# Kernel tuning notes

Measured on AMD Instinct MI355X. Metric: run time of the kernel, lower is better.

The kernel has to match this reference:

```python
import jax, jax.numpy as jnp
import numpy as np

N, E, G = 40000, 400000, 64
IN, ED, HID, HEADS, OUT = 2, 18, 64, 4, 3

def _glorot(key, shape):
    fan_in = shape[0]
    return jax.random.normal(key, shape, dtype=jnp.float32) / np.float32(np.sqrt(fan_in))

def setup_inputs():
    key = jax.random.key(0)
    ks = jax.random.split(key, 32)
    d1 = HEADS * HID  # 256
    return {
        "x": jax.random.normal(ks[0], (N, IN), jnp.float32),
        "edge_index": jax.random.randint(ks[1], (2, E), 0, N),
        "edge_attr": jax.random.normal(ks[2], (E, ED), jnp.float32),
        "batch": jnp.sort(jax.random.randint(ks[3], (N,), 0, G)),
        # conv1: TransformerConv(2 -> 64, heads=4, concat=True, beta=True, edge_dim=18)
        "Wq1": _glorot(ks[4], (IN, d1)), "bq1": jnp.zeros((d1,), jnp.float32),
        "Wk1": _glorot(ks[5], (IN, d1)), "bk1": jnp.zeros((d1,), jnp.float32),
        "Wv1": _glorot(ks[6], (IN, d1)), "bv1": jnp.zeros((d1,), jnp.float32),
        "We1": _glorot(ks[7], (ED, d1)),
        "Wskip1": _glorot(ks[8], (IN, d1)), "bskip1": jnp.zeros((d1,), jnp.float32),
        "Wbeta1": _glorot(ks[9], (3 * d1, 1)),
        # conv2: TransformerConv(256 -> 64, heads=1, concat=False, beta=True, edge_dim=18)
        "Wq2": _glorot(ks[10], (d1, HID)), "bq2": jnp.zeros((HID,), jnp.float32),
        "Wk2": _glorot(ks[11], (d1, HID)), "bk2": jnp.zeros((HID,), jnp.float32),
        "Wv2": _glorot(ks[12], (d1, HID)), "bv2": jnp.zeros((HID,), jnp.float32),
        "We2": _glorot(ks[13], (ED, HID)),
        "Wskip2": _glorot(ks[14], (d1, HID)), "bskip2": jnp.zeros((HID,), jnp.float32),
        "Wbeta2": _glorot(ks[15], (3 * HID, 1)),
        "Wlin": _glorot(ks[16], (HID, OUT)), "blin": jnp.zeros((OUT,), jnp.float32),
    }

def _tconv(x, src, dst, edge_attr, Wq, bq, Wk, bk, Wv, bv, We, Wskip, bskip, Wbeta, H, C, concat):
    # PyG TransformerConv with edge_dim, beta=True, root_weight=True (eval: dropout off)
    n = x.shape[0]
    q = (x @ Wq + bq).reshape(n, H, C)
    k = (x @ Wk + bk).reshape(n, H, C)
    v = (x @ Wv + bv).reshape(n, H, C)
    e = (edge_attr @ We).reshape(-1, H, C)              # [E,H,C]
    kj = k[src] + e                                      # key_j + edge
    alpha = jnp.einsum('ehc,ehc->eh', q[dst], kj) * (1.0 / (C ** 0.5))  # [E,H]
    # segment softmax over destination nodes
    amax = jax.ops.segment_max(alpha, dst, num_segments=n)
    ex = jnp.exp(alpha - amax[dst])
    den = jax.ops.segment_sum(ex, dst, num_segments=n)
    w = ex / (den[dst] + 1e-16)
    msg = (v[src] + e) * w[:, :, None]                   # [E,H,C]
    out = jax.ops.segment_sum(msg, dst, num_segments=n)  # [N,H,C]
    out = out.reshape(n, H * C) if concat else out.mean(axis=1)
    # beta-gated skip connection
    xr = x @ Wskip + bskip
    beta = jax.nn.sigmoid(jnp.concatenate([out, xr, out - xr], axis=-1) @ Wbeta)
    return beta * xr + (1.0 - beta) * out

def reference(x, edge_index, edge_attr, batch, Wq1, bq1, Wk1, bk1, Wv1, bv1, We1, Wskip1, bskip1, Wbeta1, Wq2, bq2, Wk2, bk2, Wv2, bv2, We2, Wskip2, bskip2, Wbeta2, Wlin, blin):
    src, dst = edge_index[0], edge_index[1]
    h = jax.nn.relu(_tconv(x, src, dst, edge_attr, Wq1, bq1, Wk1, bk1, Wv1, bv1, We1, Wskip1, bskip1, Wbeta1, HEADS, HID, True))
    h = jax.nn.relu(_tconv(h, src, dst, edge_attr, Wq2, bq2, Wk2, bk2, Wv2, bv2, We2, Wskip2, bskip2, Wbeta2, 1, HID, False))
    # global mean pool per graph
    s = jax.ops.segment_sum(h, batch, num_segments=G)
    cnt = jax.ops.segment_sum(jnp.ones((h.shape[0], 1), h.dtype), batch, num_segments=G)
    pooled = s / jnp.maximum(cnt, 1.0)
    return pooled @ Wlin + blin
```

## Files before the change

### kernel.cpp

```cpp
#include <hip/hip_runtime.h>
#include <hip/hip_fp16.h>

#define N_NODES 40000
#define N_EDGES 400000
#define N_GRAPHS 64
#define D1 256
#define HIDC 64
#define NHEADS 4
#define EDIM 18
#define EPADH 24
#define OUTF 3
#define APAD 264

typedef _Float16 f16x8 __attribute__((ext_vector_type(8)));
typedef float f32x4 __attribute__((ext_vector_type(4)));

__global__ void prep_w(const float* __restrict__ Wq, const float* __restrict__ bq,
                       const float* __restrict__ Wk, const float* __restrict__ bk,
                       const float* __restrict__ Wv, const float* __restrict__ bv,
                       const float* __restrict__ Ws, const float* __restrict__ bs,
                       const float* __restrict__ We2,
                       const float* __restrict__ Wq1, const float* __restrict__ bq1,
                       const float* __restrict__ Wk1, const float* __restrict__ bk1,
                       const float* __restrict__ We1,
                       __half* __restrict__ Bt, float* __restrict__ bias,
                       float* __restrict__ cbuf, int* __restrict__ deg) {
    int c = blockIdx.x, k = threadIdx.x;
    int gid = c * 256 + k;
    if (gid < N_NODES) deg[gid] = 0;
    if (c < 256) {
        int m = c >> 6, d = c & 63;
        const float* W = (m == 0) ? Wq : (m == 1) ? Wk : (m == 2) ? Wv : Ws;
        Bt[c * 256 + k] = __float2half(W[k * 64 + d]);
        if (k == 0) {
            const float* b = (m == 0) ? bq : (m == 1) ? bk : (m == 2) ? bv : bs;
            bias[c] = b[d];
        }
    } else if (c < 288) {
        int j = c - 256;
        float s = 0.f;
        if (j < EDIM)
            for (int cc = 0; cc < 64; ++cc) s += Wq[k * 64 + cc] * We2[j * 64 + cc];
        Bt[c * 256 + k] = __float2half(s);
        if (k == 0) {
            float b = 0.f;
            if (j < EDIM)
                for (int cc = 0; cc < 64; ++cc) b += bq[cc] * We2[j * 64 + cc];
            bias[c] = b;
        }
    } else {
        int t = k;
        if (t < 36) {
            int h = t / 9, r = t % 9, a = r / 3, b = r % 3;
            const float* A = (a == 0) ? Wq1 : (a == 1) ? Wq1 + D1 : bq1;
            const float* B = (b == 0) ? Wk1 : (b == 1) ? Wk1 + D1 : bk1;
            float s = 0.f;
            for (int cc = 0; cc < 64; ++cc) s += A[h * 64 + cc] * B[h * 64 + cc];
            cbuf[h * 63 + a * 3 + b] = s;
        } else if (t < 252) {
            int i = t - 36;
            int h = i / 54, rr = (i % 54) / 18, j = i % 18;
            const float* A = (rr == 0) ? Wq1 : (rr == 1) ? Wq1 + D1 : bq1;
            float s = 0.f;
            for (int cc = 0; cc < 64; ++cc) s += A[h * 64 + cc] * We1[j * D1 + h * 64 + cc];
            cbuf[h * 63 + 9 + rr * 18 + j] = s;
        }
    }
}

__global__ void initA(const float* __restrict__ x, const float* __restrict__ cbuf,
                      const int* __restrict__ ei, const int* __restrict__ batch,
                      float* __restrict__ coef, float* __restrict__ acc1,
                      float* __restrict__ acc2, float* __restrict__ out2,
                      int* __restrict__ deg, float* __restrict__ pooled,
                      int* __restrict__ gs, int* __restrict__ ge) {
    int t = blockIdx.x * 256 + threadIdx.x;
    acc1[t] = 0.f;
    {
        int n = t / 84, r = t % 84, h = r / 21, c = r % 21;
        const float* cb = cbuf + h * 63;
        float x0 = x[2 * n], x1 = x[2 * n + 1], o;
        if (c < 3) o = x0 * cb[c] + x1 * cb[3 + c] + cb[6 + c];
        else { int j = c - 3; o = x0 * cb[9 + j] + x1 * cb[27 + j] + cb[45 + j]; }
        coef[t] = o;
    }
    if (t < N_NODES * 64) out2[t] = 0.f;
    if (t < N_NODES * 20) acc2[t] = 0.f;
    if (t < N_EDGES) atomicAdd(&deg[ei[N_EDGES + t]], 1);
    if (t < N_GRAPHS * HIDC) pooled[t] = 0.f;
    if (t < N_NODES) {
        int b = batch[t];
        if (t == 0) gs[b] = 0;
        else { int pb = batch[t - 1]; if (pb != b) { ge[pb] = t; gs[b] = t; } }
        if (t == N_NODES - 1) ge[b] = N_NODES;
    }
}

__global__ void scanA(const int* __restrict__ deg, int* __restrict__ bsum) {
    __shared__ int s[256];
    int b = blockIdx.x, t = threadIdx.x;
    s[t] = (t < 160) ? deg[b * 160 + t] : 0;
    __syncthreads();
    for (int off = 128; off; off >>= 1) {
        if (t < off) s[t] += s[t + off];
        __syncthreads();
    }
    if (t == 0) bsum[b] = s[0];
}

__global__ void scanB(const int* __restrict__ bsum, int* __restrict__ boff) {
    __shared__ int s[256];
    int t = threadIdx.x;
    int v = (t < 250) ? bsum[t] : 0;
    s[t] = v;
    __syncthreads();
    for (int off = 1; off < 256; off <<= 1) {
        int add = (t >= off) ? s[t - off] : 0;
        __syncthreads();
        s[t] += add;
        __syncthreads();
    }
    if (t < 250) boff[t] = s[t] - v;
}

__global__ void scanC(const int* __restrict__ deg, const int* __restrict__ boff,
                      int* __restrict__ cursor) {
    __shared__ int s[256];
    int b = blockIdx.x, t = threadIdx.x;
    int v = (t < 160) ? deg[b * 160 + t] : 0;
    s[t] = v;
    __syncthreads();
    for (int off = 1; off < 256; off <<= 1) {
        int add = (t >= off) ? s[t - off] : 0;
        __syncthreads();
        s[t] += add;
        __syncthreads();
    }
    if (t < 160) cursor[b * 160 + t] = boff[b] + s[t] - v;
}

__global__ void perm_kernel(const int* __restrict__ ei, int* __restrict__ cursor,
                            int* __restrict__ inv) {
    int e = blockIdx.x * 256 + threadIdx.x;
    if (e >= N_EDGES) return;
    int p = atomicAdd(&cursor[ei[N_EDGES + e]], 1);
    inv[p] = e;
}

__global__ void gatherE(const int* __restrict__ inv, const int* __restrict__ ei,
                        const float* __restrict__ ea, const float* __restrict__ x,
                        const float* __restrict__ coef,
                        int* __restrict__ src_s, int* __restrict__ dst_s,
                        _Float16* __restrict__ eah, float* __restrict__ alpha1) {
    int p = blockIdx.x * 256 + threadIdx.x;
    if (p >= N_EDGES) return;
    int e = inv[p];
    int src = ei[e], dst = ei[N_EDGES + e];
    src_s[p] = src;
    dst_s[p] = dst;
    const float* srow = ea + (size_t)e * EDIM;
    float s[EDIM];
    #pragma unroll
    for (int j = 0; j < EDIM; ++j) s[j] = srow[j];
    float x0 = x[src * 2], x1 = x[src * 2 + 1];
    f16x8 r0 = {(_Float16)s[0], (_Float16)s[1], (_Float16)s[2], (_Float16)s[3],
                (_Float16)s[4], (_Float16)s[5], (_Float16)s[6], (_Float16)s[7]};
    f16x8 r1 = {(_Float16)s[8], (_Float16)s[9], (_Float16)s[10], (_Float16)s[11],
                (_Float16)s[12], (_Float16)s[13], (_Float16)s[14], (_Float16)s[15]};
    f16x8 r2 = {(_Float16)s[16], (_Float16)s[17], (_Float16)x0, (_Float16)x1,
                (_Float16)0.f, (_Float16)0.f, (_Float16)0.f, (_Float16)0.f};
    _Float16* drow = eah + (size_t)p * EPADH;
    *(f16x8*)(drow)      = r0;
    *(f16x8*)(drow + 8)  = r1;
    *(f16x8*)(drow + 16) = r2;
    const float* cb = coef + (size_t)dst * 84;
    #pragma unroll
    for (int h = 0; h < NHEADS; ++h) {
        const float* c = cb + h * 21;
        float a = x0 * c[0] + x1 * c[1] + c[2];
        #pragma unroll
        for (int j = 0; j < EDIM; ++j) a += s[j] * c[3 + j];
        alpha1[(size_t)h * N_EDGES + p] = __expf(a * 0.125f);
    }
}

__global__ void strip1(const int* __restrict__ dst_s, const float* __restrict__ alpha1,
                       const _Float16* __restrict__ eah, float* __restrict__ acc1) {
    int t = threadIdx.x;
    int strip = blockIdx.x * 2 + (t >> 7);
    int gl = t & 127;
    bool active = gl < 84;
    int cgl = active ? gl : 83;
    int h = cgl / 21, comp = cgl % 21;
    int voff = (comp == 0) ? 18 : (comp == 1) ? 19 : (comp - 3);
    bool isone = (comp == 2);
    int p0 = strip * 16;
    int dsts[16]; float w[16]; float v[16];
    #pragma unroll
    for (int j = 0; j < 16; ++j) dsts[j] = dst_s[p0 + j];
    #pragma unroll
    for (int j = 0; j < 16; ++j) w[j] = alpha1[(size_t)h * N_EDGES + p0 + j];
    #pragma unroll
    for (int j = 0; j < 16; ++j)
        v[j] = isone ? 1.f : (float)eah[(size_t)(p0 + j) * EPADH + voff];
    float acc = 0.f;
    int prev = dsts[0];
    #pragma unroll
    for (int j = 0; j < 16; ++j) {
        if (dsts[j] != prev) {
            if (active) atomicAdd(&acc1[(size_t)prev * 84 + gl], acc);
            acc = 0.f; prev = dsts[j];
        }
        acc += w[j] * v[j];
    }
    if (active) atomicAdd(&acc1[(size_t)prev * 84 + gl], acc);
}

__global__ void finalize1x(const float* __restrict__ x, const float* __restrict__ acc1,
                           const float* __restrict__ Wv, const float* __restrict__ bv,
                           const float* __restrict__ We, const float* __restrict__ Wskip,
                           const float* __restrict__ bskip, const float* __restrict__ Wbeta,
                           __half* __restrict__ h1f) {
    __shared__ float red[4][4];
    int nb = blockIdx.x * 4;
    int t = threadIdx.x;
    int h = t >> 6;
    float wv0 = Wv[t], wv1 = Wv[D1 + t], bvv = bv[t];
    float we[EDIM];
    #pragma unroll
    for (int j = 0; j < EDIM; ++j) we[j] = We[j * D1 + t];
    float ws0 = Wskip[t], ws1 = Wskip[D1 + t], bsv = bskip[t];
    float wb0 = Wbeta[t], wb1 = Wbeta[D1 + t], wb2 = Wbeta[2 * D1 + t];
    float o[4], xr[4], part[4];
    #pragma unroll
    for (int i = 0; i < 4; ++i) {
        int node = nb + i;
        const float* a = acc1 + (size_t)node * 84 + h * 21;
        float l = a[2];
        float oo = a[0] * wv0 + a[1] * wv1 + l * bvv;
        #pragma unroll
        for (int j = 0; j < EDIM; ++j) oo += a[3 + j] * we[j];
        oo /= (l + 1e-16f);
        float x0 = x[node * 2], x1 = x[node * 2 + 1];
        xr[i] = x0 * ws0 + x1 * ws1 + bsv;
        o[i] = oo;
        part[i] = oo * wb0 + xr[i] * wb1 + (oo - xr[i]) * wb2;
    }
    #pragma unroll
    for (int off = 32; off; off >>= 1) {
        #pragma unroll
        for (int i = 0; i < 4; ++i) part[i] += __shfl_xor(part[i], off);
    }
    if ((t & 63) == 0) {
        #pragma unroll
        for (int i = 0; i < 4; ++i) red[h][i] = part[i];
    }
    __syncthreads();
    #pragma unroll
    for (int i = 0; i < 4; ++i) {
        float tot = red[0][i] + red[1][i] + red[2][i] + red[3][i];
        float beta = 1.f / (1.f + __expf(-tot));
        h1f[(size_t)(nb + i) * D1 + t] =
            __float2half(fmaxf(beta * xr[i] + (1.f - beta) * o[i], 0.f));
    }
}

__device__ __forceinline__ void nl2_store(int c, int gr, float v,
        float* __restrict__ q2, float* __restrict__ k2, __half* __restrict__ v2h,
        float* __restrict__ xr2, float* __restrict__ qe) {
    if (c < 256) {
        int m = c >> 6, d = c & 63;
        if (m == 0)      q2[(size_t)gr * 64 + d] = v;
        else if (m == 1) k2[(size_t)gr * 64 + d] = v;
        else if (m == 2) v2h[(size_t)gr * 64 + d] = __float2half(v);
        else             xr2[(size_t)gr * 64 + d] = v;
    } else {
        qe[(size_t)gr * 32 + (c - 256)] = v;
    }
}

__global__ __launch_bounds__(256) void nl2_mfma(
        const __half* __restrict__ h1f, const __half* __restrict__ Bt,
        const float* __restrict__ bias,
        float* __restrict__ q2, float* __restrict__ k2,
        __half* __restrict__ v2h, float* __restrict__ xr2,
        float* __restrict__ qe) {
    __shared__ _Float16 As[64 * APAD];
    int t = threadIdx.x;
    int row0 = blockIdx.x * 64;
    const float4* gsrc = (const float4*)(h1f + (size_t)row0 * 256);
    #pragma unroll
    for (int i = 0; i < 8; ++i) {
        int li = i * 256 + t;
        int r = li >> 5, c8 = li & 31;
        *(float4*)(As + r * APAD + c8 * 8) = gsrc[li];
    }
    __syncthreads();
    int wave = t >> 6, lane = t & 63, quad = lane >> 4, mm = lane & 15;
    const _Float16* Bp = (const _Float16*)Bt;
    for (int ct = wave; ct < 18; ct += 4) {
        int c0 = ct * 16 + mm;
        const _Float16* b0 = Bp + (size_t)c0 * 256 + quad * 8;
        f16x8 b[8];
        #pragma unroll
        for (int s = 0; s < 8; ++s) b[s] = *(const f16x8*)(b0 + s * 32);
        float bz = bias[c0];
        #pragma unroll
        for (int rt = 0; rt < 4; ++rt) {
            const _Float16* arow = As + (rt * 16 + mm) * APAD + quad * 8;
            f16x8 a[8];
            #pragma unroll
            for (int s = 0; s < 8; ++s) a[s] = *(const f16x8*)(arow + s * 32);
            f32x4 accA = {bz, bz, bz, bz};
            f32x4 accB = {0.f, 0.f, 0.f, 0.f};
            #pragma unroll
            for (int s = 0; s < 4; ++s) {
                accA = __builtin_amdgcn_mfma_f32_16x16x32_f16(a[s],     b[s],     accA, 0, 0, 0);
                accB = __builtin_amdgcn_mfma_f32_16x16x32_f16(a[s + 4], b[s + 4], accB, 0, 0, 0);
            }
            #pragma unroll
            for (int r = 0; r < 4; ++r) {
                int gr = row0 + rt * 16 + quad * 4 + r;
                nl2_store(c0, gr, accA[r] + accB[r], q2, k2, v2h, xr2, qe);
            }
        }
    }
}

#define LG2_BLOCKS 2048
#define LG2_WAVES (LG2_BLOCKS * 4)
__global__ void logits2(const int* __restrict__ src_s, const int* __restrict__ dst_s,
                        const _Float16* __restrict__ eah, const float* __restrict__ q2,
                        const float* __restrict__ k2, const float* __restrict__ qe,
                        float* __restrict__ alpha2) {
    int t = threadIdx.x, wid = t >> 6, lane = t & 63;
    int w = blockIdx.x * 4 + wid;
    for (int base = w; base < N_EDGES; base += 2 * LG2_WAVES) {
        int p1 = base, p2 = base + LG2_WAVES;
        bool has2 = p2 < N_EDGES;
        int p2c = has2 ? p2 : p1;
        int s1 = src_s[p1], d1 = dst_s[p1];
        int s2 = src_s[p2c], d2 = dst_s[p2c];
        float dd1 = q2[(size_t)d1 * 64 + lane] * k2[(size_t)s1 * 64 + lane];
        float dd2 = q2[(size_t)d2 * 64 + lane] * k2[(size_t)s2 * 64 + lane];
        if (lane < EDIM) {
            dd1 += qe[(size_t)d1 * 32 + lane] * (float)eah[(size_t)p1 * EPADH + lane];
            dd2 += qe[(size_t)d2 * 32 + lane] * (float)eah[(size_t)p2c * EPADH + lane];
        }
        #pragma unroll
        for (int off = 32; off; off >>= 1) {
            dd1 += __shfl_xor(dd1, off);
            dd2 += __shfl_xor(dd2, off);
        }
        if (lane == 0) {
            alpha2[p1] = __expf(dd1 * 0.125f);
            if (has2) alpha2[p2] = __expf(dd2 * 0.125f);
        }
    }
}

__global__ void spmm2s(const int* __restrict__ dst_s, const int* __restrict__ src_s,
                       const float* __restrict__ alpha2, const __half* __restrict__ v2h,
                       const _Float16* __restrict__ eah,
                       float* __restrict__ out2, float* __restrict__ acc2) {
    int t = threadIdx.x;
    int strip = blockIdx.x * 4 + (t >> 6);
    int lane = t & 63;
    int p0 = strip * 16;
    int dsts[16]; int srcs[16]; float w[16];
    #pragma unroll
    for (int j = 0; j < 16; ++j) dsts[j] = dst_s[p0 + j];
    #pragma unroll
    for (int j = 0; j < 16; ++j) srcs[j] = src_s[p0 + j];
    #pragma unroll
    for (int j = 0; j < 16; ++j) w[j] = alpha2[p0 + j];
    float vv[16]; float ev[16];
    #pragma unroll
    for (int j = 0; j < 16; ++j) vv[j] = __half2float(v2h[(size_t)srcs[j] * 64 + lane]);
    #pragma unroll
    for (int j = 0; j < 16; ++j)
        ev[j] = (lane < EDIM) ? (float)eah[(size_t)(p0 + j) * EPADH + lane] : 1.f;
    float acc = 0.f, accS = 0.f;
    int prev = dsts[0];
    #pragma unroll
    for (int j = 0; j < 16; ++j) {
        if (dsts[j] != prev) {
            atomicAdd(&out2[(size_t)prev * 64 + lane], acc);
            if (lane < 19) atomicAdd(&acc2[(size_t)prev * 20 + lane], accS);
            acc = 0.f; accS = 0.f; prev = dsts[j];
        }
        acc += w[j] * vv[j];
        accS += w[j] * ev[j];
    }
    atomicAdd(&out2[(size_t)prev * 64 + lane], acc);
    if (lane < 19) atomicAdd(&acc2[(size_t)prev * 20 + lane], accS);
}

__global__ void finalize2x(const float* __restrict__ out2, const float* __restrict__ acc2,
                           const float* __restrict__ xr2, const float* __restrict__ We2,
                           const float* __restrict__ Wb2, float* __restrict__ h2) {
    __shared__ float w2s[EDIM * 64];
    int t = threadIdx.x;
    for (int i = t; i < EDIM * 64; i += 256) w2s[i] = We2[i];
    __syncthreads();
    int node = blockIdx.x * 4 + (t >> 6);
    int lane = t & 63;
    const float* a2 = acc2 + (size_t)node * 20;
    float num = out2[(size_t)node * 64 + lane];
    #pragma unroll
    for (int j = 0; j < EDIM; ++j) num += a2[j] * w2s[j * 64 + lane];
    float o = num / (a2[18] + 1e-16f);
    float xr = xr2[(size_t)node * 64 + lane];
    float part = o * Wb2[lane] + xr * Wb2[64 + lane] + (o - xr) * Wb2[128 + lane];
    #pragma unroll
    for (int off = 32; off; off >>= 1) part += __shfl_xor(part, off);
    float beta = 1.f / (1.f + __expf(-part));
    h2[(size_t)node * 64 + lane] = fmaxf(beta * xr + (1.f - beta) * o, 0.f);
}

__global__ void pool_kernel(const float* __restrict__ h2, const int* __restrict__ gs,
                            const int* __restrict__ ge, float* __restrict__ pooled) {
    __shared__ float red[4][64];
    int g = blockIdx.x >> 2, q = blockIdx.x & 3;
    int t = threadIdx.x, wv = t >> 6, lane = t & 63;
    int s = gs[g], e = ge[g];
    float sum = 0.f;
    for (int n = s + q * 4 + wv; n < e; n += 16) sum += h2[(size_t)n * 64 + lane];
    red[wv][lane] = sum;
    __syncthreads();
    if (wv == 0) {
        float v = red[0][lane] + red[1][lane] + red[2][lane] + red[3][lane];
        atomicAdd(&pooled[g * 64 + lane], v);
    }
}

__global__ void final_lin(const float* __restrict__ pooled, const int* __restrict__ gs,
                          const int* __restrict__ ge,
                          const float* __restrict__ Wlin, const float* __restrict__ blin,
                          float* __restrict__ out) {
    int t = threadIdx.x;
    if (t >= N_GRAPHS * OUTF) return;
    int g = t / OUTF, o = t % OUTF;
    int c = ge[g] - gs[g];
    float inv = 1.f / fmaxf((float)c, 1.f);
    float acc = 0.f;
    for (int kk = 0; kk < HIDC; ++kk) acc += pooled[g * 64 + kk] * Wlin[kk * OUTF + o];
    out[t] = acc * inv + blin[o];
}

extern "C" void kernel_launch(void* const* d_in, const int* in_sizes, int n_in,
                              void* d_out, int out_size, void* d_ws, size_t ws_size,
                              hipStream_t stream) {
    const float* x      = (const float*)d_in[0];
    const int*   ei     = (const int*)d_in[1];
    const float* ea     = (const float*)d_in[2];
    const int*   batch  = (const int*)d_in[3];
    const float* Wq1    = (const float*)d_in[4];  const float* bq1    = (const float*)d_in[5];
    const float* Wk1    = (const float*)d_in[6];  const float* bk1    = (const float*)d_in[7];
    const float* Wv1    = (const float*)d_in[8];  const float* bv1    = (const float*)d_in[9];
    const float* We1    = (const float*)d_in[10];
    const float* Wskip1 = (const float*)d_in[11]; const float* bskip1 = (const float*)d_in[12];
    const float* Wbeta1 = (const float*)d_in[13];
    const float* Wq2    = (const float*)d_in[14]; const float* bq2    = (const float*)d_in[15];
    const float* Wk2    = (const float*)d_in[16]; const float* bk2    = (const float*)d_in[17];
    const float* Wv2    = (const float*)d_in[18]; const float* bv2    = (const float*)d_in[19];
    const float* We2    = (const float*)d_in[20];
    const float* Wskip2 = (const float*)d_in[21]; const float* bskip2 = (const float*)d_in[22];
    const float* Wbeta2 = (const float*)d_in[23];
    const float* Wlin   = (const float*)d_in[24]; const float* blin   = (const float*)d_in[25];

    float* ptr = (float*)d_ws;
    float* q2     = ptr; ptr += (size_t)N_NODES * 64;
    float* k2     = ptr; ptr += (size_t)N_NODES * 64;
    float* xr2    = ptr; ptr += (size_t)N_NODES * 64;
    float* qe     = ptr; ptr += (size_t)N_NODES * 32;
    __half* v2h   = (__half*)ptr; ptr += (size_t)N_NODES * 32;
    _Float16* eah = (_Float16*)ptr; ptr += (size_t)N_EDGES * EPADH / 2;
    float* alpha2 = ptr; ptr += N_EDGES;
    float* acc2   = ptr; ptr += (size_t)N_NODES * 20;
    float* out2   = ptr; ptr += (size_t)N_NODES * 64;
    float* pooled = ptr; ptr += N_GRAPHS * HIDC;
    int*   gs     = (int*)ptr; ptr += N_GRAPHS;
    int*   ge     = (int*)ptr; ptr += N_GRAPHS;
    float* cbuf   = ptr; ptr += 256;
    float* bias   = ptr; ptr += 320;
    __half* Bt    = (__half*)ptr; ptr += (288 * 256) / 2;
    int*   src_s  = (int*)ptr; ptr += N_EDGES;
    int*   dst_s  = (int*)ptr; ptr += N_EDGES;
    int*   inv    = (int*)ptr; ptr += N_EDGES;
    int*   deg    = (int*)ptr; ptr += N_NODES;
    int*   cursor = (int*)ptr; ptr += N_NODES;
    int*   bsum   = (int*)ptr; ptr += 256;
    int*   boff   = (int*)ptr; ptr += 256;
    float* coef   = ptr; ptr += (size_t)N_NODES * 84;
    float* h2     = coef;
    float* acc1   = ptr; ptr += (size_t)N_NODES * 84;
    float* alpha1 = ptr; ptr += (size_t)4 * N_EDGES;
    __half* h1f   = (__half*)ptr; ptr += (size_t)N_NODES * 128;

    const int EB = (N_EDGES + 255) / 256;

    prep_w<<<289, 256, 0, stream>>>(Wq2, bq2, Wk2, bk2, Wv2, bv2, Wskip2, bskip2, We2,
                                    Wq1, bq1, Wk1, bk1, We1, Bt, bias, cbuf, deg);
    initA<<<(N_NODES * 84) / 256, 256, 0, stream>>>(x, cbuf, ei, batch, coef, acc1,
                                                    acc2, out2, deg, pooled, gs, ge);
    scanA<<<250, 256, 0, stream>>>(deg, bsum);
    scanB<<<1, 256, 0, stream>>>(bsum, boff);
    scanC<<<250, 256, 0, stream>>>(deg, boff, cursor);
    perm_kernel<<<EB, 256, 0, stream>>>(ei, cursor, inv);
    gatherE<<<EB, 256, 0, stream>>>(inv, ei, ea, x, coef, src_s, dst_s, eah, alpha1);

    strip1<<<(N_EDGES / 16) / 2, 256, 0, stream>>>(dst_s, alpha1, eah, acc1);
    finalize1x<<<N_NODES / 4, 256, 0, stream>>>(x, acc1, Wv1, bv1, We1, Wskip1, bskip1,
                                                Wbeta1, h1f);

    nl2_mfma<<<N_NODES / 64, 256, 0, stream>>>(h1f, Bt, bias, q2, k2, v2h, xr2, qe);
    logits2<<<LG2_BLOCKS, 256, 0, stream>>>(src_s, dst_s, eah, q2, k2, qe, alpha2);
    spmm2s<<<(N_EDGES / 16) / 4, 256, 0, stream>>>(dst_s, src_s, alpha2, v2h, eah,
                                                   out2, acc2);
    finalize2x<<<N_NODES / 4, 256, 0, stream>>>(out2, acc2, xr2, We2, Wbeta2, h2);

    pool_kernel<<<N_GRAPHS * 4, 256, 0, stream>>>(h2, gs, ge, pooled);
    final_lin<<<1, 256, 0, stream>>>(pooled, gs, ge, Wlin, blin, (float*)d_out);
}
```

Baseline: 457.0 us.

## Fuse edge permutation into scatter kernel and double strip length in SpMM kernels

```diff
diff --git a/kernel.cpp b/kernel.cpp
--- a/kernel.cpp
+++ b/kernel.cpp
@@ -139,23 +139,15 @@
     if (t < 160) cursor[b * 160 + t] = boff[b] + s[t] - v;
 }
 
-__global__ void perm_kernel(const int* __restrict__ ei, int* __restrict__ cursor,
-                            int* __restrict__ inv) {
+__global__ void scatterE(const int* __restrict__ ei, const float* __restrict__ ea,
+                         const float* __restrict__ x, const float* __restrict__ coef,
+                         int* __restrict__ cursor,
+                         int* __restrict__ src_s, int* __restrict__ dst_s,
+                         _Float16* __restrict__ eah, float* __restrict__ alpha1) {
     int e = blockIdx.x * 256 + threadIdx.x;
     if (e >= N_EDGES) return;
-    int p = atomicAdd(&cursor[ei[N_EDGES + e]], 1);
-    inv[p] = e;
-}
-
-__global__ void gatherE(const int* __restrict__ inv, const int* __restrict__ ei,
-                        const float* __restrict__ ea, const float* __restrict__ x,
-                        const float* __restrict__ coef,
-                        int* __restrict__ src_s, int* __restrict__ dst_s,
-                        _Float16* __restrict__ eah, float* __restrict__ alpha1) {
-    int p = blockIdx.x * 256 + threadIdx.x;
-    if (p >= N_EDGES) return;
-    int e = inv[p];
     int src = ei[e], dst = ei[N_EDGES + e];
+    int p = atomicAdd(&cursor[dst], 1);
     src_s[p] = src;
     dst_s[p] = dst;
     const float* srow = ea + (size_t)e * EDIM;
@@ -194,24 +186,28 @@
     int h = cgl / 21, comp = cgl % 21;
     int voff = (comp == 0) ? 18 : (comp == 1) ? 19 : (comp - 3);
     bool isone = (comp == 2);
-    int p0 = strip * 16;
-    int dsts[16]; float w[16]; float v[16];
-    #pragma unroll
-    for (int j = 0; j < 16; ++j) dsts[j] = dst_s[p0 + j];
-    #pragma unroll
-    for (int j = 0; j < 16; ++j) w[j] = alpha1[(size_t)h * N_EDGES + p0 + j];
-    #pragma unroll
-    for (int j = 0; j < 16; ++j)
-        v[j] = isone ? 1.f : (float)eah[(size_t)(p0 + j) * EPADH + voff];
+    int p0 = strip * 32;
     float acc = 0.f;
-    int prev = dsts[0];
-    #pragma unroll
-    for (int j = 0; j < 16; ++j) {
-        if (dsts[j] != prev) {
-            if (active) atomicAdd(&acc1[(size_t)prev * 84 + gl], acc);
-            acc = 0.f; prev = dsts[j];
-        }
-        acc += w[j] * v[j];
+    int prev = dst_s[p0];
+    #pragma unroll
+    for (int half = 0; half < 2; ++half) {
+        int q0 = p0 + half * 16;
+        int dsts[16]; float w[16]; float v[16];
+        #pragma unroll
+        for (int j = 0; j < 16; ++j) dsts[j] = dst_s[q0 + j];
+        #pragma unroll
+        for (int j = 0; j < 16; ++j) w[j] = alpha1[(size_t)h * N_EDGES + q0 + j];
+        #pragma unroll
+        for (int j = 0; j < 16; ++j)
+            v[j] = isone ? 1.f : (float)eah[(size_t)(q0 + j) * EPADH + voff];
+        #pragma unroll
+        for (int j = 0; j < 16; ++j) {
+            if (dsts[j] != prev) {
+                if (active) atomicAdd(&acc1[(size_t)prev * 84 + gl], acc);
+                acc = 0.f; prev = dsts[j];
+            }
+            acc += w[j] * v[j];
+        }
     }
     if (active) atomicAdd(&acc1[(size_t)prev * 84 + gl], acc);
 }
@@ -366,31 +362,35 @@
     int t = threadIdx.x;
     int strip = blockIdx.x * 4 + (t >> 6);
     int lane = t & 63;
-    int p0 = strip * 16;
-    int dsts[16]; int srcs[16]; float w[16];
-    #pragma unroll
-    for (int j = 0; j < 16; ++j) dsts[j] = dst_s[p0 + j];
-    #pragma unroll
-    for (int j = 0; j < 16; ++j) srcs[j] = src_s[p0 + j];
-    #pragma unroll
-    for (int j = 0; j < 16; ++j) w[j] = alpha2[p0 + j];
-    float vv[16]; float ev[16];
-    #pragma unroll
-    for (int j = 0; j < 16; ++j) vv[j] = __half2float(v2h[(size_t)srcs[j] * 64 + lane]);
-    #pragma unroll
-    for (int j = 0; j < 16; ++j)
-        ev[j] = (lane < EDIM) ? (float)eah[(size_t)(p0 + j) * EPADH + lane] : 1.f;
+    int p0 = strip * 32;
     float acc = 0.f, accS = 0.f;
-    int prev = dsts[0];
-    #pragma unroll
-    for (int j = 0; j < 16; ++j) {
-        if (dsts[j] != prev) {
-            atomicAdd(&out2[(size_t)prev * 64 + lane], acc);
-            if (lane < 19) atomicAdd(&acc2[(size_t)prev * 20 + lane], accS);
-            acc = 0.f; accS = 0.f; prev = dsts[j];
-        }
-        acc += w[j] * vv[j];
-        accS += w[j] * ev[j];
+    int prev = dst_s[p0];
+    #pragma unroll
+    for (int half = 0; half < 2; ++half) {
+        int q0 = p0 + half * 16;
+        int dsts[16]; int srcs[16]; float w[16];
+        #pragma unroll
+        for (int j = 0; j < 16; ++j) dsts[j] = dst_s[q0 + j];
+        #pragma unroll
+        for (int j = 0; j < 16; ++j) srcs[j] = src_s[q0 + j];
+        #pragma unroll
+        for (int j = 0; j < 16; ++j) w[j] = alpha2[q0 + j];
+        float vv[16]; float ev[16];
+        #pragma unroll
+        for (int j = 0; j < 16; ++j) vv[j] = __half2float(v2h[(size_t)srcs[j] * 64 + lane]);
+        #pragma unroll
+        for (int j = 0; j < 16; ++j)
+            ev[j] = (lane < EDIM) ? (float)eah[(size_t)(q0 + j) * EPADH + lane] : 1.f;
+        #pragma unroll
+        for (int j = 0; j < 16; ++j) {
+            if (dsts[j] != prev) {
+                atomicAdd(&out2[(size_t)prev * 64 + lane], acc);
+                if (lane < 19) atomicAdd(&acc2[(size_t)prev * 20 + lane], accS);
+                acc = 0.f; accS = 0.f; prev = dsts[j];
+            }
+            acc += w[j] * vv[j];
+            accS += w[j] * ev[j];
+        }
     }
     atomicAdd(&out2[(size_t)prev * 64 + lane], acc);
     if (lane < 19) atomicAdd(&acc2[(size_t)prev * 20 + lane], accS);
@@ -487,7 +487,6 @@
     __half* Bt    = (__half*)ptr; ptr += (288 * 256) / 2;
     int*   src_s  = (int*)ptr; ptr += N_EDGES;
     int*   dst_s  = (int*)ptr; ptr += N_EDGES;
-    int*   inv    = (int*)ptr; ptr += N_EDGES;
     int*   deg    = (int*)ptr; ptr += N_NODES;
     int*   cursor = (int*)ptr; ptr += N_NODES;
     int*   bsum   = (int*)ptr; ptr += 256;
@@ -507,16 +506,15 @@
     scanA<<<250, 256, 0, stream>>>(deg, bsum);
     scanB<<<1, 256, 0, stream>>>(bsum, boff);
     scanC<<<250, 256, 0, stream>>>(deg, boff, cursor);
-    perm_kernel<<<EB, 256, 0, stream>>>(ei, cursor, inv);
-    gatherE<<<EB, 256, 0, stream>>>(inv, ei, ea, x, coef, src_s, dst_s, eah, alpha1);
-
-    strip1<<<(N_EDGES / 16) / 2, 256, 0, stream>>>(dst_s, alpha1, eah, acc1);
+    scatterE<<<EB, 256, 0, stream>>>(ei, ea, x, coef, cursor, src_s, dst_s, eah, alpha1);
+
+    strip1<<<(N_EDGES / 32) / 2, 256, 0, stream>>>(dst_s, alpha1, eah, acc1);
     finalize1x<<<N_NODES / 4, 256, 0, stream>>>(x, acc1, Wv1, bv1, We1, Wskip1, bskip1,
                                                 Wbeta1, h1f);
 
     nl2_mfma<<<N_NODES / 64, 256, 0, stream>>>(h1f, Bt, bias, q2, k2, v2h, xr2, qe);
     logits2<<<LG2_BLOCKS, 256, 0, stream>>>(src_s, dst_s, eah, q2, k2, qe, alpha2);
-    spmm2s<<<(N_EDGES / 16) / 4, 256, 0, stream>>>(dst_s, src_s, alpha2, v2h, eah,
+    spmm2s<<<(N_EDGES / 32) / 4, 256, 0, stream>>>(dst_s, src_s, alpha2, v2h, eah,
                                                    out2, acc2);
     finalize2x<<<N_NODES / 4, 256, 0, stream>>>(out2, acc2, xr2, We2, Wbeta2, h2);
 
```

Result: slower. 531.2 us (+16.2%).
